# Optimization experiments

Measured on AMD Instinct MI355X. Metric: run time of the kernel, lower is better.

## Reference

```python
import jax, jax.numpy as jnp
from jax import lax
import numpy as np

KK = 9  # 3x3 deformable kernel taps


def conv3x3(x, w, b):
    # x [N,C,H,W], w [O,I,3,3] (OIHW), stride 1, pad 1
    y = lax.conv_general_dilated(x, w, (1, 1), 'SAME',
                                 dimension_numbers=('NCHW', 'OIHW', 'NCHW'))
    return y + b[None, :, None, None]


def prelu(x, a):
    return jnp.where(x >= 0, x, a[None, :, None, None] * x)


def dcn(feat, offset, mask, w, b):
    # Modulated deformable conv (DCNv2), kernel 3x3, stride 1, pad 1, dg=1.
    # feat [N,C,H,W], offset [N,2*KK,H,W] (channel 2k = dy_k, 2k+1 = dx_k),
    # mask [N,KK,H,W], w [O,C,3,3].
    N, C, H, W = feat.shape
    O = w.shape[0]
    ky, kx = jnp.meshgrid(jnp.arange(3), jnp.arange(3), indexing='ij')
    ky = (ky - 1).reshape(KK).astype(feat.dtype)  # dilation 1, pad 1
    kx = (kx - 1).reshape(KK).astype(feat.dtype)
    off = offset.reshape(N, KK, 2, H, W)
    yy = jnp.arange(H, dtype=feat.dtype)[:, None]
    xx = jnp.arange(W, dtype=feat.dtype)[None, :]
    py = yy[None, None] + ky[None, :, None, None] + off[:, :, 0]  # [N,KK,H,W]
    px = xx[None, None] + kx[None, :, None, None] + off[:, :, 1]
    y0 = jnp.floor(py)
    x0 = jnp.floor(px)
    wy = py - y0
    wx = px - x0
    y0i = y0.astype(jnp.int32)
    x0i = x0.astype(jnp.int32)
    feat_flat = feat.reshape(N, C, H * W)

    def gather(yi, xi):
        valid = (yi >= 0) & (yi < H) & (xi >= 0) & (xi < W)
        yc = jnp.clip(yi, 0, H - 1)
        xc = jnp.clip(xi, 0, W - 1)
        idx = (yc * W + xc).reshape(N, 1, KK * H * W)
        g = jnp.take_along_axis(feat_flat, jnp.broadcast_to(idx, (N, C, KK * H * W)), axis=2)
        g = g.reshape(N, C, KK, H, W)
        return g * valid[:, None].astype(feat.dtype)

    v = (gather(y0i, x0i) * ((1 - wy) * (1 - wx))[:, None]
         + gather(y0i, x0i + 1) * ((1 - wy) * wx)[:, None]
         + gather(y0i + 1, x0i) * (wy * (1 - wx))[:, None]
         + gather(y0i + 1, x0i + 1) * (wy * wx)[:, None])  # [N,C,KK,H,W]
    v = v * mask[:, None]
    out = jnp.einsum('nckhw,ock->nohw', v, w.reshape(O, C, KK))
    return out + b[None, :, None, None]


def setup_inputs() -> dict:
    key = jax.random.key(0)
    ks = jax.random.split(key, 8)
    B, T, C, H, W = 8, 5, 3, 64, 64
    F = 64

    def winit(k, shape, fan_in, scale=1.0):
        return jax.random.normal(k, shape, jnp.float32) * (scale / np.sqrt(fan_in))

    return {
        'x': jax.random.normal(ks[0], (B, T, C, H, W), jnp.float32),
        'flow': jnp.zeros((T, B, 2, H, W), jnp.float32),  # unused (use_flow=False)
        'W_init': winit(ks[1], (F, C, 3, 3), C * 9),
        'b_init': jnp.zeros((F,), jnp.float32),
        'a_init': jnp.full((F,), 0.25, jnp.float32),
        'W_off': winit(ks[2], (F, 2 * C, 3, 3), 2 * C * 9),
        'b_off': jnp.zeros((F,), jnp.float32),
        'a_off': jnp.full((F,), 0.25, jnp.float32),
        'W_om': winit(ks[3], (3 * KK, F, 3, 3), F * 9, scale=0.1),  # small offsets
        'b_om': jnp.zeros((3 * KK,), jnp.float32),
        'W_dcn': winit(ks[4], (F, F, 3, 3), F * 9),
        'b_dcn': jnp.zeros((F,), jnp.float32),
    }


def reference(x, flow, W_init, b_init, a_init, W_off, b_off, a_off,
              W_om, b_om, W_dcn, b_dcn):
    B, T, C, H, W = x.shape
    xf = x.reshape(B * T, C, H, W)
    # per-frame feature extraction (batched over frames)
    feat = prelu(conv3x3(xf, W_init, b_init), a_init)             # [BT,F,H,W]
    # offset features from (reference frame 0, frame j) pairs
    ref0 = jnp.broadcast_to(x[:, :1], x.shape).reshape(B * T, C, H, W)
    pair = jnp.concatenate([ref0, xf], axis=1)                    # [BT,2C,H,W]
    off_feat = prelu(conv3x3(pair, W_off, b_off), a_off)          # [BT,F,H,W]
    # DCNv2 offset/mask head
    om = conv3x3(off_feat, W_om, b_om)                            # [BT,27,H,W]
    o1, o2, m = jnp.split(om, 3, axis=1)
    offset = jnp.concatenate([o1, o2], axis=1)                    # [BT,18,H,W]
    mask = jax.nn.sigmoid(m)                                      # [BT,9,H,W]
    out = dcn(feat, offset, mask, W_dcn, b_dcn)                   # [BT,F,H,W]
    return out.reshape(B, T, -1, H, W)
```

## Files before the change

### kernel.cpp

```cpp
#include <hip/hip_runtime.h>
#include <hip/hip_fp16.h>
#include <stdint.h>

typedef __attribute__((ext_vector_type(8))) _Float16 f16x8;
typedef __attribute__((ext_vector_type(4))) float f32x4;

#define NIMG 40
#define TFR  5
#define CIN  3
#define HH   64
#define WW   64
#define HW   4096
#define PPS  72
#define RSTR 72
#define CSTR 144

union U32H2 { uint u; __half2 h; };

__device__ __forceinline__ ushort4 f4_to_h4(f32x4 a) {
  ushort4 r;
  r.x = __half_as_ushort(__float2half(a[0]));
  r.y = __half_as_ushort(__float2half(a[1]));
  r.z = __half_as_ushort(__float2half(a[2]));
  r.w = __half_as_ushort(__float2half(a[3]));
  return r;
}
__device__ __forceinline__ void h4_add(f32x4& a, ushort4 s) {
  a[0] += __half2float(__ushort_as_half(s.x));
  a[1] += __half2float(__ushort_as_half(s.y));
  a[2] += __half2float(__ushort_as_half(s.z));
  a[3] += __half2float(__ushort_as_half(s.w));
}

__global__ __launch_bounds__(256) void k_wprep(
    const float* __restrict__ Wd, const float* __restrict__ Wom,
    const float* __restrict__ Wi, const float* __restrict__ Wo,
    __half* __restrict__ Waf, __half* __restrict__ Womf,
    __half* __restrict__ Wff, __half* __restrict__ Wof)
{
  int idx = blockIdx.x*256 + threadIdx.x;
  if (idx < 36864) {
    int j = idx & 7, lane = (idx >> 3) & 63;
    int grp = idx >> 9;
    int ot = grp & 3, tg = grp >> 2;
    int tap = tg % 9, kg = tg / 9;
    int row = lane & 15, ks = lane >> 4;
    int oc = ot*16 + row;
    int c  = kg*32 + ks*8 + j;
    Waf[idx] = __float2half(Wd[oc*576 + c*9 + tap]);
  } else if (idx < 36864 + 18432) {
    int q = idx - 36864;
    int j = q & 7, lane = (q >> 3) & 63;
    int grp = q >> 9;
    int k0 = grp % 18, mt = grp / 18;
    int row = lane & 15, ks = lane >> 4;
    int oc = mt*16 + row;
    int tap = k0 >> 1;
    int c = (k0 & 1)*32 + ks*8 + j;
    Womf[q] = (oc < 27) ? __float2half(Wom[oc*576 + c*9 + tap]) : __float2half(0.f);
  } else if (idx < 36864 + 18432 + 2048) {
    int q = idx - 36864 - 18432;
    int j = q & 7, lane = (q >> 3) & 63;
    int wv = q >> 9;
    int row = lane & 15, ks = lane >> 4;
    int f = wv*16 + row;
    int kk = ks*8 + j;
    Wff[q] = (kk < 27) ? __float2half(Wi[f*27 + kk]) : __float2half(0.f);
  } else if (idx < 36864 + 18432 + 2048 + 4096) {
    int q = idx - 36864 - 18432 - 2048;
    int j = q & 7, lane = (q >> 3) & 63;
    int grp = q >> 9;
    int wv = grp >> 1, half = grp & 1;
    int row = lane & 15, ks = lane >> 4;
    int f = wv*16 + row;
    int kk = half*32 + ks*8 + j;
    float v = 0.f;
    if (kk < 27)       v = Wo[f*54 + 27 + kk];
    else if (kk < 54)  v = Wo[f*54 + (kk - 27)];
    Wof[q] = __float2half(v);
  }
}

__global__ __launch_bounds__(256) void k_front(
    const float* __restrict__ x,
    const __half* __restrict__ Wff, const __half* __restrict__ Wof,
    const float* __restrict__ bi, const float* __restrict__ ai,
    const float* __restrict__ bo, const float* __restrict__ aof,
    __half* __restrict__ feat, __half* __restrict__ offf)
{
  __shared__ __align__(16) __half sp[32*PPS];
  int t = threadIdx.x, blk = blockIdx.x;
  int n = blk >> 7;
  int pbase = (blk & 127) * 32;
  int h = pbase >> 6;
  int wbase = pbase & 63;
  int n0 = (n/TFR)*TFR;
  const float* xc = x + (size_t)n*(CIN*HW);
  const float* xr = x + (size_t)n0*(CIN*HW);

  #pragma unroll
  for (int i = 0; i < 8; ++i) {
    int e = i*256 + t;
    int kk = e >> 5, px = e & 31;
    float v = 0.f;
    if (kk < 54) {
      int cur = (kk < 27);
      int kb = cur ? kk : kk - 27;
      int c = kb / 9, k = kb - c*9;
      int y  = h + k/3 - 1;
      int xx = wbase + px + (k - (k/3)*3) - 1;
      if (y >= 0 && y < HH && xx >= 0 && xx < WW)
        v = (cur ? xc : xr)[c*HW + y*WW + xx];
    }
    sp[px*PPS + kk] = __float2half(v);
  }
  __syncthreads();

  int wv = t >> 6, lane = t & 63;
  int row = lane & 15, ks = lane >> 4;
  f16x8 af0 = *(const f16x8*)(Wff + (wv<<9) + lane*8);
  f16x8 aw0 = *(const f16x8*)(Wof + (wv<<10) + lane*8);
  f16x8 aw1 = *(const f16x8*)(Wof + (wv<<10) + 512 + lane*8);
  #pragma unroll
  for (int nt = 0; nt < 2; ++nt) {
    const __half* bp = sp + (nt*16 + row)*PPS + ks*8;
    f16x8 b0 = *(const f16x8*)(bp);
    f16x8 b1 = *(const f16x8*)(bp + 32);
    f32x4 accf = {0.f,0.f,0.f,0.f}, acco = {0.f,0.f,0.f,0.f};
    accf = __builtin_amdgcn_mfma_f32_16x16x32_f16(af0, b0, accf, 0, 0, 0);
    acco = __builtin_amdgcn_mfma_f32_16x16x32_f16(aw0, b0, acco, 0, 0, 0);
    acco = __builtin_amdgcn_mfma_f32_16x16x32_f16(aw1, b1, acco, 0, 0, 0);
    int p  = pbase + nt*16 + row;
    int f0 = wv*16 + ks*4;
    size_t base = ((size_t)n*HW + p)*64 + f0;
    union { ushort4 u; __half b[4]; } pf, po;
    #pragma unroll
    for (int j = 0; j < 4; ++j) {
      float vf = accf[j] + bi[f0+j];
      float aF = ai[f0+j];
      vf = vf >= 0.f ? vf : aF*vf;
      pf.b[j] = __float2half(vf);
      float vo = acco[j] + bo[f0+j];
      float aO = aof[f0+j];
      vo = vo >= 0.f ? vo : aO*vo;
      po.b[j] = __float2half(vo);
    }
    *(ushort4*)(feat + base) = pf.u;
    *(ushort4*)(offf + base) = po.u;
  }
}

__global__ __launch_bounds__(512, 8) void k_dcn(
    const __half* __restrict__ feat, const __half* __restrict__ offf,
    const __half* __restrict__ Waf, const __half* __restrict__ Womf,
    const float* __restrict__ bom, const float* __restrict__ bd,
    float* __restrict__ out)
{
  __shared__ __align__(16) char smem[5*36*CSTR];
  __shared__ __align__(16) char smem2[6912];
  __shared__ __half som[27*36];
  __shared__ int sflag;
  ushort4* soff = (ushort4*)smem2;
  uint4*   swgt = (uint4*)(smem2 + 2304);
  __half*  mbuf = (__half*)smem2;

  int t = threadIdx.x;
  int blk = blockIdx.x;
  int work = (blk & 7)*640 + (blk >> 3);
  int n = work >> 7;
  int pbase = (work & 127) * 32;
  int hrow = pbase >> 6, wbase = pbase & 63;
  int wv = t >> 6, lane = t & 63;
  int row = lane & 15, ks = lane >> 4;
  int nt = wv & 1, kg = (wv >> 1) & 1, oh = wv >> 2;
  int pxl = nt*16 + row;
  int cb = kg*64 + ks*16;

  const char* ob = (const char*)(offf + (size_t)n*(HW*64));
  const char* fb = (const char*)(feat + (size_t)n*(HW*64));
  __half* region = (__half*)smem;
  char* sfeat = smem;

  if (t == 0) sflag = 1;

  uint4 wreg0 = make_uint4(0,0,0,0), wreg1 = wreg0, wreg2 = wreg0;
  {
    int u0 = t, u1 = 512 + t, u2 = 1024 + t;
    {
      int r = u0 / 288, rem = u0 - r*288, ci = rem >> 3, q = rem & 7;
      int y = hrow - 2 + r, xx = wbase - 2 + ci;
      if ((unsigned)y < 64u && (unsigned)xx < 64u)
        wreg0 = *(const uint4*)(fb + (((y<<6)+xx)<<7) + q*16);
    }
    {
      int r = u1 / 288, rem = u1 - r*288, ci = rem >> 3, q = rem & 7;
      int y = hrow - 2 + r, xx = wbase - 2 + ci;
      if ((unsigned)y < 64u && (unsigned)xx < 64u)
        wreg1 = *(const uint4*)(fb + (((y<<6)+xx)<<7) + q*16);
    }
    if (u2 < 1440) {
      int r = u2 / 288, rem = u2 - r*288, ci = rem >> 3, q = rem & 7;
      int y = hrow - 2 + r, xx = wbase - 2 + ci;
      if ((unsigned)y < 64u && (unsigned)xx < 64u)
        wreg2 = *(const uint4*)(fb + (((y<<6)+xx)<<7) + q*16);
    }
  }

  for (int u = t; u < 816; u += 512) {
    int ry = u / 272;
    int rem = u - ry*272;
    int rx = rem >> 3, q = rem & 7;
    int y = hrow + ry - 1, xx = wbase + rx - 1;
    uint4 v = make_uint4(0,0,0,0);
    if ((unsigned)y < 64u && (unsigned)xx < 64u)
      v = *(const uint4*)(ob + (((y<<6)+xx)<<7) + q*16);
    *(uint4*)((char*)region + ((ry*34 + rx)*RSTR + q*8)*2) = v;
  }
  __syncthreads();

  if (kg == 0) {
    int mt = oh;
    f32x4 acc = {0.f,0.f,0.f,0.f};
    #pragma unroll
    for (int k0 = 0; k0 < 18; ++k0) {
      int k = k0 >> 1, ky = k/3, kx = k - ky*3;
      int c0 = (k0 & 1)*32;
      f16x8 a = *(const f16x8*)(Womf + ((mt*18 + k0)<<9) + lane*8);
      f16x8 b = *(const f16x8*)(region + (ky*34 + pxl + kx)*RSTR + c0 + ks*8);
      acc = __builtin_amdgcn_mfma_f32_16x16x32_f16(a, b, acc, 0, 0, 0);
    }
    #pragma unroll
    for (int j = 0; j < 4; ++j) {
      int oc = mt*16 + ks*4 + j;
      if (oc < 27) {
        float r = acc[j] + bom[oc];
        if (oc >= 18) r = 1.f/(1.f + __expf(-r));
        som[oc*36 + pxl] = __float2half(r);
      }
    }
  }
  __syncthreads();

  {
    int u0 = t, u1 = 512 + t, u2 = 1024 + t;
    {
      int r = u0 / 288, rem = u0 - r*288, ci = rem >> 3, q = rem & 7;
      *(uint4*)(sfeat + (r*36 + ci)*CSTR + q*16) = wreg0;
    }
    {
      int r = u1 / 288, rem = u1 - r*288, ci = rem >> 3, q = rem & 7;
      *(uint4*)(sfeat + (r*36 + ci)*CSTR + q*16) = wreg1;
    }
    if (u2 < 1440) {
      int r = u2 / 288, rem = u2 - r*288, ci = rem >> 3, q = rem & 7;
      *(uint4*)(sfeat + (r*36 + ci)*CSTR + q*16) = wreg2;
    }
  }

  if (t < 288) {
    int e = t;
    int px = e / 9, k = e - px*9;
    int w = wbase + px;
    float dy = __half2float(som[(2*k)*36 + px]);
    float dx = __half2float(som[(2*k+1)*36 + px]);
    float m  = __half2float(som[(18+k)*36 + px]);
    float py = (float)(hrow + (k/3) - 1) + dy;
    float qx = (float)(w + (k - (k/3)*3) - 1) + dx;
    float y0f = floorf(py), x0f = floorf(qx);
    float wy = py - y0f, wx = qx - x0f;
    int y0 = (int)y0f, x0 = (int)x0f;
    int y1 = y0 + 1, x1 = x0 + 1;
    float w00 = (1.f-wy)*(1.f-wx)*m;
    float w01 = (1.f-wy)*wx*m;
    float w10 = wy*(1.f-wx)*m;
    float w11 = wy*wx*m;
    if (y0 < 0 || y0 >= HH) { w00 = 0.f; w01 = 0.f; }
    if (y1 < 0 || y1 >= HH) { w10 = 0.f; w11 = 0.f; }
    if (x0 < 0 || x0 >= WW) { w00 = 0.f; w10 = 0.f; }
    if (x1 < 0 || x1 >= WW) { w01 = 0.f; w11 = 0.f; }
    int y0c = min(max(y0,0),HH-1), y1c = min(max(y1,0),HH-1);
    int x0c = min(max(x0,0),WW-1), x1c = min(max(x1,0),WW-1);
    int yw0 = y0c - (hrow-2), yw1 = y1c - (hrow-2);
    int xw0 = x0c - (wbase-2), xw1 = x1c - (wbase-2);
    bool ok = ((unsigned)yw0 < 5u) & ((unsigned)yw1 < 5u)
            & ((unsigned)xw0 < 36u) & ((unsigned)xw1 < 36u);
    if (!ok) atomicAnd(&sflag, 0);
    int cy0 = min(max(yw0,0),4), cy1 = min(max(yw1,0),4);
    int cx0 = min(max(xw0,0),35), cx1 = min(max(xw1,0),35);
    soff[e] = make_ushort4((ushort)((cy0*36 + cx0)*CSTR), (ushort)((cy0*36 + cx1)*CSTR),
                           (ushort)((cy1*36 + cx0)*CSTR), (ushort)((cy1*36 + cx1)*CSTR));
    U32H2 u00, u01, u10, u11;
    u00.h = __float2half2_rn(w00); u01.h = __float2half2_rn(w01);
    u10.h = __float2half2_rn(w10); u11.h = __float2half2_rn(w11);
    swgt[e] = make_uint4(u00.u, u01.u, u10.u, u11.u);
  }
  __syncthreads();

  f32x4 acc0 = {0.f,0.f,0.f,0.f}, acc1 = {0.f,0.f,0.f,0.f};
  const __half* afrag = Waf + (kg*9)*2048 + (oh*2)*512 + lane*8;

  if (sflag) {
    #pragma unroll
    for (int tap = 0; tap < 9; ++tap) {
      int e = pxl*9 + tap;
      ushort4 off = soff[e];
      uint4 wq  = swgt[e];
      U32H2 W00, W01, W10, W11;
      W00.u = wq.x; W01.u = wq.y; W10.u = wq.z; W11.u = wq.w;
      uint4 c00 = *(const uint4*)(sfeat + (int)off.x + cb);
      uint4 c01 = *(const uint4*)(sfeat + (int)off.y + cb);
      uint4 c10 = *(const uint4*)(sfeat + (int)off.z + cb);
      uint4 c11 = *(const uint4*)(sfeat + (int)off.w + cb);
      uint4 r;
#define BILIN(comp) { U32H2 a0v,a1v,a2v,a3v,res;                                \
      a0v.u = c00.comp; a1v.u = c01.comp; a2v.u = c10.comp; a3v.u = c11.comp;   \
      __half2 v = __hmul2(W00.h, a0v.h); v = __hfma2(W01.h, a1v.h, v);          \
      v = __hfma2(W10.h, a2v.h, v);      v = __hfma2(W11.h, a3v.h, v);          \
      res.h = v; r.comp = res.u; }
      BILIN(x) BILIN(y) BILIN(z) BILIN(w)
      f16x8 b = *(f16x8*)&r;
      const __half* ap = afrag + tap*2048;
      f16x8 a0 = *(const f16x8*)(ap);
      f16x8 a1 = *(const f16x8*)(ap + 512);
      acc0 = __builtin_amdgcn_mfma_f32_16x16x32_f16(a0, b, acc0, 0, 0, 0);
      acc1 = __builtin_amdgcn_mfma_f32_16x16x32_f16(a1, b, acc1, 0, 0, 0);
    }
  } else {
    #pragma unroll 1
    for (int tap = 0; tap < 9; ++tap) {
      float dy = __half2float(som[(2*tap)*36 + pxl]);
      float dx = __half2float(som[(2*tap+1)*36 + pxl]);
      float m  = __half2float(som[(18+tap)*36 + pxl]);
      int ky = tap/3, kx = tap - ky*3;
      float py = (float)(hrow + ky - 1) + dy;
      float qx = (float)(wbase + pxl + kx - 1) + dx;
      float y0f = floorf(py), x0f = floorf(qx);
      float wy = py - y0f, wx = qx - x0f;
      int y0 = (int)y0f, x0 = (int)x0f;
      int y1 = y0 + 1, x1 = x0 + 1;
      float w00 = (1.f-wy)*(1.f-wx)*m;
      float w01 = (1.f-wy)*wx*m;
      float w10 = wy*(1.f-wx)*m;
      float w11 = wy*wx*m;
      if (y0 < 0 || y0 >= HH) { w00 = 0.f; w01 = 0.f; }
      if (y1 < 0 || y1 >= HH) { w10 = 0.f; w11 = 0.f; }
      if (x0 < 0 || x0 >= WW) { w00 = 0.f; w10 = 0.f; }
      if (x1 < 0 || x1 >= WW) { w01 = 0.f; w11 = 0.f; }
      int y0c = min(max(y0,0),HH-1), y1c = min(max(y1,0),HH-1);
      int x0c = min(max(x0,0),WW-1), x1c = min(max(x1,0),WW-1);
      int o00 = (((y0c<<6)+x0c)<<7), o01 = (((y0c<<6)+x1c)<<7);
      int o10 = (((y1c<<6)+x0c)<<7), o11 = (((y1c<<6)+x1c)<<7);
      U32H2 W00, W01, W10, W11;
      W00.h = __float2half2_rn(w00); W01.h = __float2half2_rn(w01);
      W10.h = __float2half2_rn(w10); W11.h = __float2half2_rn(w11);
      uint4 c00 = *(const uint4*)(fb + o00 + cb);
      uint4 c01 = *(const uint4*)(fb + o01 + cb);
      uint4 c10 = *(const uint4*)(fb + o10 + cb);
      uint4 c11 = *(const uint4*)(fb + o11 + cb);
      uint4 r;
      BILIN(x) BILIN(y) BILIN(z) BILIN(w)
#undef BILIN
      f16x8 b = *(f16x8*)&r;
      const __half* ap = afrag + tap*2048;
      f16x8 a0 = *(const f16x8*)(ap);
      f16x8 a1 = *(const f16x8*)(ap + 512);
      acc0 = __builtin_amdgcn_mfma_f32_16x16x32_f16(a0, b, acc0, 0, 0, 0);
      acc1 = __builtin_amdgcn_mfma_f32_16x16x32_f16(a1, b, acc1, 0, 0, 0);
    }
  }
  __syncthreads();

  if (kg == 1) {
    int mb = pxl*72 + oh*32 + ks*4;
    *(ushort4*)(mbuf + mb)      = f4_to_h4(acc0);
    *(ushort4*)(mbuf + mb + 16) = f4_to_h4(acc1);
  }
  __syncthreads();
  if (kg == 0) {
    int mb = pxl*72 + oh*32 + ks*4;
    h4_add(acc0, *(ushort4*)(mbuf + mb));
    h4_add(acc1, *(ushort4*)(mbuf + mb + 16));
    int p = pbase + pxl;
    float* op = out + (size_t)n*(64*HW) + p;
    #pragma unroll
    for (int j = 0; j < 4; ++j) {
      int oc = oh*32 + ks*4 + j;
      op[(oc     )*HW] = acc0[j] + bd[oc];
      op[(oc + 16)*HW] = acc1[j] + bd[oc + 16];
    }
  }
}

extern "C" void kernel_launch(void* const* d_in, const int* in_sizes, int n_in,
                              void* d_out, int out_size, void* d_ws, size_t ws_size,
                              hipStream_t stream)
{
  const float* x   = (const float*)d_in[0];
  const float* Wi  = (const float*)d_in[2];
  const float* bi  = (const float*)d_in[3];
  const float* ai  = (const float*)d_in[4];
  const float* Wo  = (const float*)d_in[5];
  const float* bo  = (const float*)d_in[6];
  const float* aof = (const float*)d_in[7];
  const float* Wom = (const float*)d_in[8];
  const float* bom = (const float*)d_in[9];
  const float* Wd  = (const float*)d_in[10];
  const float* bd  = (const float*)d_in[11];
  float* out = (float*)d_out;

  __half* feat = (__half*)d_ws;
  __half* offf = feat + (size_t)NIMG*HW*64;
  __half* Waf  = offf + (size_t)NIMG*HW*64;
  __half* Womf = Waf + 36864;
  __half* Wff  = Womf + 18432;
  __half* Wof  = Wff + 2048;

  hipLaunchKernelGGL(k_wprep, dim3(240),         dim3(256), 0, stream,
                     Wd, Wom, Wi, Wo, Waf, Womf, Wff, Wof);
  hipLaunchKernelGGL(k_front, dim3(NIMG*HW/32),  dim3(256), 0, stream,
                     x, Wff, Wof, bi, ai, bo, aof, feat, offf);
  hipLaunchKernelGGL(k_dcn,   dim3(NIMG*HW/32),  dim3(512), 0, stream,
                     feat, offf, Waf, Womf, bom, bd, out);
}
```

Baseline: 96.41 us.

## Split DCN taps across wave groups so each wave computes all output channels

Instead of splitting the 64 output channels across the upper and lower wave halves, each wave now computes all four 16-channel output tiles and the halves split the 9 taps (5 and 4). Each bilinear-interpolated B fragment is reused for four MFMAs rather than two, so the gather and interpolation work per wave drops by about half. The cost is a larger cross-wave reduction: three partial slabs go through shared memory (enlarged smem2) in fp16, more accumulator registers, and an uneven 5/4 tap split.

```diff
diff --git a/kernel.cpp b/kernel.cpp
--- a/kernel.cpp
+++ b/kernel.cpp
@@ -14,6 +14,8 @@
 #define PPS  72
 #define RSTR 72
 #define CSTR 144
+#define SOMS 34
+#define MBS  68
 
 union U32H2 { uint u; __half2 h; };
 
@@ -30,6 +32,101 @@
   a[1] += __half2float(__ushort_as_half(s.y));
   a[2] += __half2float(__ushort_as_half(s.z));
   a[3] += __half2float(__ushort_as_half(s.w));
+}
+
+__device__ __forceinline__ uint4 bilin4(uint4 c00, uint4 c01, uint4 c10, uint4 c11, uint4 wq) {
+  U32H2 W00, W01, W10, W11;
+  W00.u = wq.x; W01.u = wq.y; W10.u = wq.z; W11.u = wq.w;
+  uint4 r;
+#define BILIN(comp) { U32H2 a0v,a1v,a2v,a3v,res;                                \
+  a0v.u = c00.comp; a1v.u = c01.comp; a2v.u = c10.comp; a3v.u = c11.comp;       \
+  __half2 v = __hmul2(W00.h, a0v.h); v = __hfma2(W01.h, a1v.h, v);              \
+  v = __hfma2(W10.h, a2v.h, v);      v = __hfma2(W11.h, a3v.h, v);              \
+  res.h = v; r.comp = res.u; }
+  BILIN(x) BILIN(y) BILIN(z) BILIN(w)
+#undef BILIN
+  return r;
+}
+
+template<int T0, int T1>
+__device__ __forceinline__ void dcn_taps_fast(
+    const char* sfeat, const ushort4* soff, const uint4* swgt,
+    const __half* afrag, int pxl, int cb,
+    f32x4& acc0, f32x4& acc1, f32x4& acc2, f32x4& acc3)
+{
+  #pragma unroll
+  for (int tap = T0; tap < T1; ++tap) {
+    int e = pxl*9 + tap;
+    ushort4 off = soff[e];
+    uint4 wq  = swgt[e];
+    uint4 c00 = *(const uint4*)(sfeat + (int)off.x + cb);
+    uint4 c01 = *(const uint4*)(sfeat + (int)off.y + cb);
+    uint4 c10 = *(const uint4*)(sfeat + (int)off.z + cb);
+    uint4 c11 = *(const uint4*)(sfeat + (int)off.w + cb);
+    uint4 r = bilin4(c00, c01, c10, c11, wq);
+    f16x8 b = *(f16x8*)&r;
+    const __half* ap = afrag + tap*2048;
+    f16x8 a0 = *(const f16x8*)(ap);
+    f16x8 a1 = *(const f16x8*)(ap + 512);
+    f16x8 a2 = *(const f16x8*)(ap + 1024);
+    f16x8 a3 = *(const f16x8*)(ap + 1536);
+    acc0 = __builtin_amdgcn_mfma_f32_16x16x32_f16(a0, b, acc0, 0, 0, 0);
+    acc1 = __builtin_amdgcn_mfma_f32_16x16x32_f16(a1, b, acc1, 0, 0, 0);
+    acc2 = __builtin_amdgcn_mfma_f32_16x16x32_f16(a2, b, acc2, 0, 0, 0);
+    acc3 = __builtin_amdgcn_mfma_f32_16x16x32_f16(a3, b, acc3, 0, 0, 0);
+  }
+}
+
+template<int T0, int T1>
+__device__ __forceinline__ void dcn_taps_slow(
+    const __half* som, const char* fb, const __half* afrag,
+    int pxl, int cb, int hrow, int wbase,
+    f32x4& acc0, f32x4& acc1, f32x4& acc2, f32x4& acc3)
+{
+  #pragma unroll 1
+  for (int tap = T0; tap < T1; ++tap) {
+    float dy = __half2float(som[(2*tap)*SOMS + pxl]);
+    float dx = __half2float(som[(2*tap+1)*SOMS + pxl]);
+    float m  = __half2float(som[(18+tap)*SOMS + pxl]);
+    int ky = tap/3, kx = tap - ky*3;
+    float py = (float)(hrow + ky - 1) + dy;
+    float qx = (float)(wbase + pxl + kx - 1) + dx;
+    float y0f = floorf(py), x0f = floorf(qx);
+    float wy = py - y0f, wx = qx - x0f;
+    int y0 = (int)y0f, x0 = (int)x0f;
+    int y1 = y0 + 1, x1 = x0 + 1;
+    float w00 = (1.f-wy)*(1.f-wx)*m;
+    float w01 = (1.f-wy)*wx*m;
+    float w10 = wy*(1.f-wx)*m;
+    float w11 = wy*wx*m;
+    if (y0 < 0 || y0 >= HH) { w00 = 0.f; w01 = 0.f; }
+    if (y1 < 0 || y1 >= HH) { w10 = 0.f; w11 = 0.f; }
+    if (x0 < 0 || x0 >= WW) { w00 = 0.f; w10 = 0.f; }
+    if (x1 < 0 || x1 >= WW) { w01 = 0.f; w11 = 0.f; }
+    int y0c = min(max(y0,0),HH-1), y1c = min(max(y1,0),HH-1);
+    int x0c = min(max(x0,0),WW-1), x1c = min(max(x1,0),WW-1);
+    int o00 = (((y0c<<6)+x0c)<<7), o01 = (((y0c<<6)+x1c)<<7);
+    int o10 = (((y1c<<6)+x0c)<<7), o11 = (((y1c<<6)+x1c)<<7);
+    U32H2 u00, u01, u10, u11;
+    u00.h = __float2half2_rn(w00); u01.h = __float2half2_rn(w01);
+    u10.h = __float2half2_rn(w10); u11.h = __float2half2_rn(w11);
+    uint4 wq = make_uint4(u00.u, u01.u, u10.u, u11.u);
+    uint4 c00 = *(const uint4*)(fb + o00 + cb);
+    uint4 c01 = *(const uint4*)(fb + o01 + cb);
+    uint4 c10 = *(const uint4*)(fb + o10 + cb);
+    uint4 c11 = *(const uint4*)(fb + o11 + cb);
+    uint4 r = bilin4(c00, c01, c10, c11, wq);
+    f16x8 b = *(f16x8*)&r;
+    const __half* ap = afrag + tap*2048;
+    f16x8 a0 = *(const f16x8*)(ap);
+    f16x8 a1 = *(const f16x8*)(ap + 512);
+    f16x8 a2 = *(const f16x8*)(ap + 1024);
+    f16x8 a3 = *(const f16x8*)(ap + 1536);
+    acc0 = __builtin_amdgcn_mfma_f32_16x16x32_f16(a0, b, acc0, 0, 0, 0);
+    acc1 = __builtin_amdgcn_mfma_f32_16x16x32_f16(a1, b, acc1, 0, 0, 0);
+    acc2 = __builtin_amdgcn_mfma_f32_16x16x32_f16(a2, b, acc2, 0, 0, 0);
+    acc3 = __builtin_amdgcn_mfma_f32_16x16x32_f16(a3, b, acc3, 0, 0, 0);
+  }
 }
 
 __global__ __launch_bounds__(256) void k_wprep(
@@ -157,8 +254,8 @@
     float* __restrict__ out)
 {
   __shared__ __align__(16) char smem[5*36*CSTR];
-  __shared__ __align__(16) char smem2[6912];
-  __shared__ __half som[27*36];
+  __shared__ __align__(16) char smem2[13056];
+  __shared__ __half som[27*SOMS];
   __shared__ int sflag;
   ushort4* soff = (ushort4*)smem2;
   uint4*   swgt = (uint4*)(smem2 + 2304);
@@ -172,7 +269,7 @@
   int hrow = pbase >> 6, wbase = pbase & 63;
   int wv = t >> 6, lane = t & 63;
   int row = lane & 15, ks = lane >> 4;
-  int nt = wv & 1, kg = (wv >> 1) & 1, oh = wv >> 2;
+  int nt = wv & 1, kg = (wv >> 1) & 1, tg = wv >> 2;
   int pxl = nt*16 + row;
   int cb = kg*64 + ks*16;
 
@@ -219,7 +316,7 @@
   __syncthreads();
 
   if (kg == 0) {
-    int mt = oh;
+    int mt = tg;
     f32x4 acc = {0.f,0.f,0.f,0.f};
     #pragma unroll
     for (int k0 = 0; k0 < 18; ++k0) {
@@ -235,7 +332,7 @@
       if (oc < 27) {
         float r = acc[j] + bom[oc];
         if (oc >= 18) r = 1.f/(1.f + __expf(-r));
-        som[oc*36 + pxl] = __float2half(r);
+        som[oc*SOMS + pxl] = __float2half(r);
       }
     }
   }
@@ -261,9 +358,9 @@
     int e = t;
     int px = e / 9, k = e - px*9;
     int w = wbase + px;
-    float dy = __half2float(som[(2*k)*36 + px]);
-    float dx = __half2float(som[(2*k+1)*36 + px]);
-    float m  = __half2float(som[(18+k)*36 + px]);
+    float dy = __half2float(som[(2*k)*SOMS + px]);
+    float dx = __half2float(som[(2*k+1)*SOMS + px]);
+    float m  = __half2float(som[(18+k)*SOMS + px]);
     float py = (float)(hrow + (k/3) - 1) + dy;
     float qx = (float)(w + (k - (k/3)*3) - 1) + dx;
     float y0f = floorf(py), x0f = floorf(qx);
@@ -297,96 +394,44 @@
   __syncthreads();
 
   f32x4 acc0 = {0.f,0.f,0.f,0.f}, acc1 = {0.f,0.f,0.f,0.f};
-  const __half* afrag = Waf + (kg*9)*2048 + (oh*2)*512 + lane*8;
-
+  f32x4 acc2 = {0.f,0.f,0.f,0.f}, acc3 = {0.f,0.f,0.f,0.f};
+  const __half* afrag = Waf + (kg*9)*2048 + lane*8;
   if (sflag) {
-    #pragma unroll
-    for (int tap = 0; tap < 9; ++tap) {
-      int e = pxl*9 + tap;
-      ushort4 off = soff[e];
-      uint4 wq  = swgt[e];
-      U32H2 W00, W01, W10, W11;
-      W00.u = wq.x; W01.u = wq.y; W10.u = wq.z; W11.u = wq.w;
-      uint4 c00 = *(const uint4*)(sfeat + (int)off.x + cb);
-      uint4 c01 = *(const uint4*)(sfeat + (int)off.y + cb);
-      uint4 c10 = *(const uint4*)(sfeat + (int)off.z + cb);
-      uint4 c11 = *(const uint4*)(sfeat + (int)off.w + cb);
-      uint4 r;
-#define BILIN(comp) { U32H2 a0v,a1v,a2v,a3v,res;                                \
-      a0v.u = c00.comp; a1v.u = c01.comp; a2v.u = c10.comp; a3v.u = c11.comp;   \
-      __half2 v = __hmul2(W00.h, a0v.h); v = __hfma2(W01.h, a1v.h, v);          \
-      v = __hfma2(W10.h, a2v.h, v);      v = __hfma2(W11.h, a3v.h, v);          \
-      res.h = v; r.comp = res.u; }
-      BILIN(x) BILIN(y) BILIN(z) BILIN(w)
-      f16x8 b = *(f16x8*)&r;
-      const __half* ap = afrag + tap*2048;
-      f16x8 a0 = *(const f16x8*)(ap);
-      f16x8 a1 = *(const f16x8*)(ap + 512);
-      acc0 = __builtin_amdgcn_mfma_f32_16x16x32_f16(a0, b, acc0, 0, 0, 0);
-      acc1 = __builtin_amdgcn_mfma_f32_16x16x32_f16(a1, b, acc1, 0, 0, 0);
-    }
+    if (tg == 0) dcn_taps_fast<0,5>(sfeat, soff, swgt, afrag, pxl, cb, acc0, acc1, acc2, acc3);
+    else         dcn_taps_fast<5,9>(sfeat, soff, swgt, afrag, pxl, cb, acc0, acc1, acc2, acc3);
   } else {
-    #pragma unroll 1
-    for (int tap = 0; tap < 9; ++tap) {
-      float dy = __half2float(som[(2*tap)*36 + pxl]);
-      float dx = __half2float(som[(2*tap+1)*36 + pxl]);
-      float m  = __half2float(som[(18+tap)*36 + pxl]);
-      int ky = tap/3, kx = tap - ky*3;
-      float py = (float)(hrow + ky - 1) + dy;
-      float qx = (float)(wbase + pxl + kx - 1) + dx;
-      float y0f = floorf(py), x0f = floorf(qx);
-      float wy = py - y0f, wx = qx - x0f;
-      int y0 = (int)y0f, x0 = (int)x0f;
-      int y1 = y0 + 1, x1 = x0 + 1;
-      float w00 = (1.f-wy)*(1.f-wx)*m;
-      float w01 = (1.f-wy)*wx*m;
-      float w10 = wy*(1.f-wx)*m;
-      float w11 = wy*wx*m;
-      if (y0 < 0 || y0 >= HH) { w00 = 0.f; w01 = 0.f; }
-      if (y1 < 0 || y1 >= HH) { w10 = 0.f; w11 = 0.f; }
-      if (x0 < 0 || x0 >= WW) { w00 = 0.f; w10 = 0.f; }
-      if (x1 < 0 || x1 >= WW) { w01 = 0.f; w11 = 0.f; }
-      int y0c = min(max(y0,0),HH-1), y1c = min(max(y1,0),HH-1);
-      int x0c = min(max(x0,0),WW-1), x1c = min(max(x1,0),WW-1);
-      int o00 = (((y0c<<6)+x0c)<<7), o01 = (((y0c<<6)+x1c)<<7);
-      int o10 = (((y1c<<6)+x0c)<<7), o11 = (((y1c<<6)+x1c)<<7);
-      U32H2 W00, W01, W10, W11;
-      W00.h = __float2half2_rn(w00); W01.h = __float2half2_rn(w01);
-      W10.h = __float2half2_rn(w10); W11.h = __float2half2_rn(w11);
-      uint4 c00 = *(const uint4*)(fb + o00 + cb);
-      uint4 c01 = *(const uint4*)(fb + o01 + cb);
-      uint4 c10 = *(const uint4*)(fb + o10 + cb);
-      uint4 c11 = *(const uint4*)(fb + o11 + cb);
-      uint4 r;
-      BILIN(x) BILIN(y) BILIN(z) BILIN(w)
-#undef BILIN
-      f16x8 b = *(f16x8*)&r;
-      const __half* ap = afrag + tap*2048;
-      f16x8 a0 = *(const f16x8*)(ap);
-      f16x8 a1 = *(const f16x8*)(ap + 512);
-      acc0 = __builtin_amdgcn_mfma_f32_16x16x32_f16(a0, b, acc0, 0, 0, 0);
-      acc1 = __builtin_amdgcn_mfma_f32_16x16x32_f16(a1, b, acc1, 0, 0, 0);
-    }
-  }
-  __syncthreads();
-
-  if (kg == 1) {
-    int mb = pxl*72 + oh*32 + ks*4;
+    if (tg == 0) dcn_taps_slow<0,5>(som, fb, afrag, pxl, cb, hrow, wbase, acc0, acc1, acc2, acc3);
+    else         dcn_taps_slow<5,9>(som, fb, afrag, pxl, cb, hrow, wbase, acc0, acc1, acc2, acc3);
+  }
+  __syncthreads();
+
+  int slab = kg*2 + tg - 1;
+  if (wv >= 2 || tg == 1) {
+    int mb = slab*(32*MBS) + pxl*MBS + ks*4;
     *(ushort4*)(mbuf + mb)      = f4_to_h4(acc0);
     *(ushort4*)(mbuf + mb + 16) = f4_to_h4(acc1);
-  }
-  __syncthreads();
-  if (kg == 0) {
-    int mb = pxl*72 + oh*32 + ks*4;
-    h4_add(acc0, *(ushort4*)(mbuf + mb));
-    h4_add(acc1, *(ushort4*)(mbuf + mb + 16));
+    *(ushort4*)(mbuf + mb + 32) = f4_to_h4(acc2);
+    *(ushort4*)(mbuf + mb + 48) = f4_to_h4(acc3);
+  }
+  __syncthreads();
+  if (kg == 0 && tg == 0) {
+    int mb = pxl*MBS + ks*4;
+    #pragma unroll
+    for (int s = 0; s < 3; ++s) {
+      h4_add(acc0, *(ushort4*)(mbuf + s*(32*MBS) + mb));
+      h4_add(acc1, *(ushort4*)(mbuf + s*(32*MBS) + mb + 16));
+      h4_add(acc2, *(ushort4*)(mbuf + s*(32*MBS) + mb + 32));
+      h4_add(acc3, *(ushort4*)(mbuf + s*(32*MBS) + mb + 48));
+    }
     int p = pbase + pxl;
     float* op = out + (size_t)n*(64*HW) + p;
     #pragma unroll
     for (int j = 0; j < 4; ++j) {
-      int oc = oh*32 + ks*4 + j;
+      int oc = ks*4 + j;
       op[(oc     )*HW] = acc0[j] + bd[oc];
       op[(oc + 16)*HW] = acc1[j] + bd[oc + 16];
+      op[(oc + 32)*HW] = acc2[j] + bd[oc + 32];
+      op[(oc + 48)*HW] = acc3[j] + bd[oc + 48];
     }
   }
 }
```

Result: faster. 90.92 us (-5.7%).
